# Kernel optimization log

Measured on AMD Instinct MI355X. Metric: run time of the kernel, lower is better.

Reference implementation:

```python
import jax, jax.numpy as jnp
import numpy as np
import math

MUL = 32
E = 131072
N = 10000
IRREPS = [(0, 1), (1, -1), (2, 1)]  # (l, parity) for 0e + 1o + 2e
SQRT3 = math.sqrt(3.0)

_f = math.factorial


def _w3j_symbol(j1, j2, j3, m1, m2, m3):
    """Standard (complex-basis) Wigner 3j symbol via the Racah formula."""
    if m1 + m2 + m3 != 0:
        return 0.0
    if abs(m1) > j1 or abs(m2) > j2 or abs(m3) > j3:
        return 0.0
    if not (abs(j1 - j2) <= j3 <= j1 + j2):
        return 0.0
    tri = _f(j1 + j2 - j3) * _f(j1 - j2 + j3) * _f(-j1 + j2 + j3) / _f(j1 + j2 + j3 + 1)
    pref = (-1) ** (j1 - j2 - m3) * math.sqrt(
        tri * _f(j1 + m1) * _f(j1 - m1) * _f(j2 + m2) * _f(j2 - m2) * _f(j3 + m3) * _f(j3 - m3)
    )
    tmin = max(0, j2 - j3 - m1, j1 - j3 + m2)
    tmax = min(j1 + j2 - j3, j1 - m1, j2 + m2)
    s = 0.0
    for t in range(tmin, tmax + 1):
        s += (-1) ** t / (
            _f(t) * _f(j3 - j2 + t + m1) * _f(j3 - j1 + t - m2)
            * _f(j1 + j2 - j3 - t) * _f(j1 - t - m1) * _f(j2 - t + m2)
        )
    return pref * s


def _real_basis(l):
    """Complex -> real spherical-harmonic change of basis, rows m=-l..l."""
    U = np.zeros((2 * l + 1, 2 * l + 1), dtype=np.complex128)
    U[l, l] = 1.0
    s = 1.0 / math.sqrt(2.0)
    for m in range(1, l + 1):
        U[l + m, l + m] = ((-1) ** m) * s
        U[l + m, l - m] = s
        U[l - m, l - m] = 1j * s
        U[l - m, l + m] = -1j * ((-1) ** m) * s
    return U


def _w3j_real(l1, l2, l3):
    """Real-basis Wigner 3j tensor, Frobenius norm 1 (e3nn normalization)."""
    Wc = np.zeros((2 * l1 + 1, 2 * l2 + 1, 2 * l3 + 1), dtype=np.complex128)
    for m1 in range(-l1, l1 + 1):
        for m2 in range(-l2, l2 + 1):
            for m3 in range(-l3, l3 + 1):
                Wc[l1 + m1, l2 + m2, l3 + m3] = _w3j_symbol(l1, l2, l3, m1, m2, m3)
    C = np.einsum('im,jn,ko,mno->ijk', _real_basis(l1), _real_basis(l2), _real_basis(l3), Wc)
    re, im = C.real, C.imag
    R = re if np.linalg.norm(re) >= np.linalg.norm(im) else im
    return R / np.linalg.norm(R)


def _build_w3j():
    dims = [2 * l + 1 for l, _ in IRREPS]
    offs = np.concatenate([[0], np.cumsum(dims)])[:-1]
    base_dim = int(sum(dims))  # 9
    # auto-generated instructions: same loop order as the torch module
    ins = []
    for io, (lo, po) in enumerate(IRREPS):
        for i1, (l1, p1) in enumerate(IRREPS):
            for i2, (l2, p2) in enumerate(IRREPS):
                if p1 * p2 == po and abs(l1 - l2) <= lo <= l1 + l2:
                    ins.append((i1, i2, io))
    P = len(ins)  # 11 paths
    w3j = np.zeros((P, base_dim, base_dim, base_dim), dtype=np.float32)
    for p, (i1, i2, io) in enumerate(ins):
        l1, l2, lo = IRREPS[i1][0], IRREPS[i2][0], IRREPS[io][0]
        C = _w3j_real(l1, l2, lo) * math.sqrt(2 * lo + 1)  # component normalization
        w3j[p, offs[i1]:offs[i1] + dims[i1], offs[i2]:offs[i2] + dims[i2], offs[io]:offs[io] + dims[io]] = C
    return w3j


def setup_inputs() -> dict:
    key = jax.random.key(0)
    k1, k2, k3, k4 = jax.random.split(key, 4)
    w3j = jnp.asarray(_build_w3j())  # [P=11, 9, 9, 9]
    P = w3j.shape[0]
    base_dim = w3j.shape[1]
    return {
        'x1': jax.random.normal(k1, (E, MUL * base_dim), dtype=jnp.float32),
        'x2': jax.random.normal(k2, (E, MUL * base_dim), dtype=jnp.float32),
        'idxs': jax.random.randint(k3, (E,), 0, N),
        'weights': jax.random.uniform(k4, (MUL, P), dtype=jnp.float32, minval=-SQRT3, maxval=SQRT3),
        'w3j': w3j,
        'scatter_dim_size': N,
    }


def reference(x1, x2, idxs, weights, w3j, scatter_dim_size):
    base1 = w3j.shape[1]
    base2 = w3j.shape[2]
    # scatter edges -> nodes, then gather back per edge (neighbor sum per center)
    x2s = jax.ops.segment_sum(x2, idxs, num_segments=int(scatter_dim_size))
    x2g = x2s[idxs]
    x1r = x1.reshape(-1, MUL, base1)   # [E, u, i]
    x2r = x2g.reshape(-1, MUL, base2)  # [E, u, j]
    # path-channel coupled weighting: 'up,pijk->uijk'
    ww3j = jnp.einsum('up,pijk->uijk', weights, w3j)
    # out[e,u,k] = sum_ij x1[e,u,i] x2[e,u,j] ww3j[u,i,j,k]
    out = jnp.einsum('eui,euj,uijk->euk', x1r, x2r, ww3j)
    return out
```

## Files before the change

### kernel.cpp

```cpp
#include <hip/hip_runtime.h>

#define MULV 32
#define BASE 9
#define ROW 288
#define NPATH 11
#define W3J_SZ 729
#define PACK_STRIDE 96
#define PACK_TOTAL (MULV * PACK_STRIDE)
#define TILE 64
#define BLK 512
#define HCOL 144
#define LSTR 145
#define NH4 36
#define HTOT (TILE * NH4)

typedef float f4a4 __attribute__((ext_vector_type(4), aligned(4)));

__device__ constexpr int p_o1[NPATH] = {0,1,4, 0,1,1,4, 0,1,4,4};
__device__ constexpr int p_d1[NPATH] = {1,3,5, 1,3,3,5, 1,3,5,5};
__device__ constexpr int p_o2[NPATH] = {0,1,4, 1,0,4,1, 4,1,0,4};
__device__ constexpr int p_d2[NPATH] = {1,3,5, 3,1,5,3, 5,3,1,5};
__device__ constexpr int p_o3[NPATH] = {0,0,0, 1,1,1,1, 4,4,4,4};
__device__ constexpr int p_d3[NPATH] = {1,1,1, 3,3,3,3, 5,5,5,5};
__device__ constexpr int p_l1[NPATH] = {0,1,2, 0,1,1,2, 0,1,2,2};
__device__ constexpr int p_l2[NPATH] = {0,1,2, 1,0,2,1, 2,1,0,2};
__device__ constexpr int p_l3[NPATH] = {0,0,0, 1,1,1,1, 2,2,2,2};

__device__ __host__ constexpr bool cell_nz(int p, int i, int j, int k) {
    int m1 = i - p_l1[p], m2 = j - p_l2[p], m3 = k - p_l3[p];
    if ((((m1 < 0) + (m2 < 0) + (m3 < 0)) & 1) != 0) return false;
    int a1 = m1 < 0 ? -m1 : m1, a2 = m2 < 0 ? -m2 : m2, a3 = m3 < 0 ? -m3 : m3;
    int d = a1 - a2; if (d < 0) d = -d;
    return (a3 == a1 + a2) || (a3 == d);
}
__device__ __host__ constexpr bool pair_nz(int p, int i, int j) {
    for (int k = 0; k < p_d3[p]; ++k) if (cell_nz(p, i, j, k)) return true;
    return false;
}


__global__ void zero_count_kernel(float* __restrict__ ws, const int* __restrict__ dN) {
    int N = dN[0];
    int* count = (int*)(ws + PACK_TOTAL + (long)N * ROW);
    for (int i = blockIdx.x * blockDim.x + threadIdx.x; i < N; i += gridDim.x * blockDim.x)
        count[i] = 0;
}

__global__ void hist_kernel(const int* __restrict__ idxs, float* __restrict__ ws,
                            const int* __restrict__ dN, int E) {
    int N = dN[0];
    int* count = (int*)(ws + PACK_TOTAL + (long)N * ROW);
    int t = blockIdx.x * blockDim.x + threadIdx.x;
    if (t < E) atomicAdd(&count[idxs[t]], 1);
}

__global__ void scan_kernel(float* __restrict__ ws, const int* __restrict__ dN) {
    int N = dN[0];
    int* count  = (int*)(ws + PACK_TOTAL + (long)N * ROW);
    int* offset = count + N;
    int* cursor = count + 2 * N;
    __shared__ int tsum[1024];
    const int tid = threadIdx.x;
    int cpt = (N + 1023) / 1024;
    int lo = tid * cpt;
    int hi = lo + cpt; if (hi > N) hi = N;
    int s = 0;
    for (int i = lo; i < hi; ++i) s += count[i];
    int v = s;
    tsum[tid] = v;
    __syncthreads();
    #pragma unroll
    for (int off = 1; off < 1024; off <<= 1) {
        int t = (tid >= off) ? tsum[tid - off] : 0;
        __syncthreads();
        v += t;
        tsum[tid] = v;
        __syncthreads();
    }
    int run = v - s;
    for (int i = lo; i < hi; ++i) {
        int c = count[i];
        offset[i] = run; cursor[i] = run;
        run += c;
    }
}

__global__ void fill_kernel(const int* __restrict__ idxs, float* __restrict__ ws,
                            const int* __restrict__ dN, int E) {
    int N = dN[0];
    int* count  = (int*)(ws + PACK_TOTAL + (long)N * ROW);
    int* cursor = count + 2 * N;
    int* bucket = count + 3 * N;
    int t = blockIdx.x * blockDim.x + threadIdx.x;
    if (t < E) {
        int n = idxs[t];
        int pos = atomicAdd(&cursor[n], 1);
        bucket[pos] = t;
    }
}

__global__ __launch_bounds__(256) void gather_sum_kernel(const float* __restrict__ x2,
                                                         float* __restrict__ ws,
                                                         const int* __restrict__ dN) {
    int N = dN[0];
    float* x2s  = ws + PACK_TOTAL;
    int* count  = (int*)(x2s + (long)N * ROW);
    int* offset = count + N;
    int* bucket = count + 3 * N;
    const int lane = threadIdx.x & 63;
    const int wv   = threadIdx.x >> 6;
    for (int n0 = blockIdx.x * 4 + wv; n0 < N; n0 += gridDim.x * 4) {
        int n   = __builtin_amdgcn_readfirstlane(n0);
        int off = offset[n];
        int deg = count[n];
        float4 a0 = make_float4(0.f, 0.f, 0.f, 0.f);
        float4 a1 = make_float4(0.f, 0.f, 0.f, 0.f);
        int d = 0;
        for (; d + 4 <= deg; d += 4) {
            int e0 = bucket[off + d + 0];
            int e1 = bucket[off + d + 1];
            int e2 = bucket[off + d + 2];
            int e3 = bucket[off + d + 3];
            const float4* r0 = (const float4*)(x2 + (long)e0 * ROW);
            const float4* r1 = (const float4*)(x2 + (long)e1 * ROW);
            const float4* r2 = (const float4*)(x2 + (long)e2 * ROW);
            const float4* r3 = (const float4*)(x2 + (long)e3 * ROW);
            float4 v0 = r0[lane], v1 = r1[lane], v2 = r2[lane], v3 = r3[lane];
            float4 w0, w1, w2, w3;
            if (lane < 8) {
                w0 = r0[64 + lane]; w1 = r1[64 + lane];
                w2 = r2[64 + lane]; w3 = r3[64 + lane];
            }
            a0.x += v0.x + v1.x + v2.x + v3.x;
            a0.y += v0.y + v1.y + v2.y + v3.y;
            a0.z += v0.z + v1.z + v2.z + v3.z;
            a0.w += v0.w + v1.w + v2.w + v3.w;
            if (lane < 8) {
                a1.x += w0.x + w1.x + w2.x + w3.x;
                a1.y += w0.y + w1.y + w2.y + w3.y;
                a1.z += w0.z + w1.z + w2.z + w3.z;
                a1.w += w0.w + w1.w + w2.w + w3.w;
            }
        }
        for (; d < deg; ++d) {
            int e = bucket[off + d];
            const float4* row = (const float4*)(x2 + (long)e * ROW);
            float4 v = row[lane];
            a0.x += v.x; a0.y += v.y; a0.z += v.z; a0.w += v.w;
            if (lane < 8) {
                float4 w = row[64 + lane];
                a1.x += w.x; a1.y += w.y; a1.z += w.z; a1.w += w.w;
            }
        }
        float4* orow = (float4*)(x2s + (long)n * ROW);
        orow[lane] = a0;
        if (lane < 8) orow[64 + lane] = a1;
    }
}

__global__ void ww_build_kernel(const float* __restrict__ weights,
                                const float* __restrict__ w3j,
                                float* __restrict__ packed) {
    int u = threadIdx.x;
    if (u >= MULV) return;
    int ci = 0;
    #pragma unroll
    for (int p = 0; p < NPATH; ++p) {
        float wgt = weights[u * NPATH + p];
        #pragma unroll
        for (int i = 0; i < p_d1[p]; ++i)
            #pragma unroll
            for (int j = 0; j < p_d2[p]; ++j)
                #pragma unroll
                for (int k = 0; k < p_d3[p]; ++k)
                    if (cell_nz(p, i, j, k)) {
                        int idx = (p_o1[p] + i) * 81 + (p_o2[p] + j) * 9 + (p_o3[p] + k);
                        packed[u * PACK_STRIDE + ci] = wgt * w3j[p * W3J_SZ + idx];
                        ++ci;
                    }
    }
}

template <bool GUARD>
__global__ __launch_bounds__(512, 4) void contract_kernel(
    const float* __restrict__ x1, const int* __restrict__ idxs,
    float* __restrict__ ws, const int* __restrict__ dN,
    float* __restrict__ out, int E)
{
    __shared__ float tile[TILE * LSTR];
    __shared__ int lperm[TILE];
    const int tid = threadIdx.x;
    const long ebase = (long)blockIdx.x * TILE;
    const float* __restrict__ packed = ws;
    const float* __restrict__ x2s    = ws + PACK_TOTAL;
    const int N = dN[0];
    const int* __restrict__ bucket = (const int*)(x2s + (long)N * ROW) + 3 * N;

    if (tid < TILE) {
        long ee = ebase + tid;
        lperm[tid] = (!GUARD || ee < (long)E) ? bucket[ee] : -1;
    }
    __syncthreads();

    const int lane = tid & 63;
    const int wv   = __builtin_amdgcn_readfirstlane(tid >> 6);
    const int e    = lperm[lane];
    const int n    = idxs[e >= 0 ? e : 0];
    const float* __restrict__ r2 = x2s + n * ROW;
    float* __restrict__ lrow = &tile[lane * LSTR];

    float x2c[BASE];
    {
        const float* s = r2 + wv * BASE;
        f4a4 a = *(const f4a4*)s;
        f4a4 b = *(const f4a4*)(s + 4);
        x2c[0]=a.x; x2c[1]=a.y; x2c[2]=a.z; x2c[3]=a.w;
        x2c[4]=b.x; x2c[5]=b.y; x2c[6]=b.z; x2c[7]=b.w;
        x2c[8]=s[8];
    }

    #pragma unroll 1
    for (int h = 0; h < 2; ++h) {
        for (int q = tid; q < HTOT; q += BLK) {
            int r = q / NH4, c = q - r * NH4;
            int er = lperm[r];
            if (!GUARD || er >= 0) {
                float4 v = *(const float4*)(x1 + (long)er * ROW + h * HCOL + c * 4);
                float* d = &tile[r * LSTR + c * 4];
                d[0] = v.x; d[1] = v.y; d[2] = v.z; d[3] = v.w;
            }
        }
        __syncthreads();

        #pragma unroll 1
        for (int cc = 0; cc < 2; ++cc) {
            const int m = 2 * h + cc;
            const int u = m * 8 + wv;
            const float* __restrict__ wp = packed + u * PACK_STRIDE;

            float x2n[BASE];
            if (m < 3) {
                const float* s = r2 + (u + 8) * BASE;
                f4a4 a = *(const f4a4*)s;
                f4a4 b = *(const f4a4*)(s + 4);
                x2n[0]=a.x; x2n[1]=a.y; x2n[2]=a.z; x2n[3]=a.w;
                x2n[4]=b.x; x2n[5]=b.y; x2n[6]=b.z; x2n[7]=b.w;
                x2n[8]=s[8];
            }

            const int lbase = (cc * 8 + wv) * BASE;
            float x1v[BASE], acc[BASE];
            #pragma unroll
            for (int i = 0; i < BASE; ++i) {
                x1v[i] = lrow[lbase + i];
                acc[i] = 0.0f;
            }

            int ci = 0;
            #pragma unroll
            for (int p = 0; p < NPATH; ++p) {
                #pragma unroll
                for (int i = 0; i < p_d1[p]; ++i) {
                    #pragma unroll
                    for (int j = 0; j < p_d2[p]; ++j) {
                        if (pair_nz(p, i, j)) {
                            float xx = x1v[p_o1[p] + i] * x2c[p_o2[p] + j];
                            #pragma unroll
                            for (int k = 0; k < p_d3[p]; ++k) {
                                if (cell_nz(p, i, j, k)) {
                                    acc[p_o3[p] + k] = fmaf(wp[ci], xx, acc[p_o3[p] + k]);
                                    ++ci;
                                }
                            }
                        }
                    }
                }
            }
            #pragma unroll
            for (int k = 0; k < BASE; ++k)
                lrow[lbase + k] = acc[k];
            if (m < 3) {
                #pragma unroll
                for (int i = 0; i < BASE; ++i) x2c[i] = x2n[i];
            }
        }
        __syncthreads();

        for (int q = tid; q < HTOT; q += BLK) {
            int r = q / NH4, c = q - r * NH4;
            int er = lperm[r];
            if (!GUARD || er >= 0) {
                const float* s = &tile[r * LSTR + c * 4];
                *(float4*)(out + (long)er * ROW + h * HCOL + c * 4) =
                    make_float4(s[0], s[1], s[2], s[3]);
            }
        }
    }
}

extern "C" void kernel_launch(void* const* d_in, const int* in_sizes, int n_in,
                              void* d_out, int out_size, void* d_ws, size_t ws_size,
                              hipStream_t stream) {
    const float* x1      = (const float*)d_in[0];
    const float* x2      = (const float*)d_in[1];
    const int*   idxs    = (const int*)d_in[2];
    const float* weights = (const float*)d_in[3];
    const float* w3j     = (const float*)d_in[4];
    const int*   dN      = (const int*)d_in[5];
    float* out = (float*)d_out;
    float* ws  = (float*)d_ws;

    const int E = in_sizes[2];
    const int eb = (E + 255) / 256;

    zero_count_kernel<<<256, 256, 0, stream>>>(ws, dN);
    hist_kernel<<<eb, 256, 0, stream>>>(idxs, ws, dN, E);
    scan_kernel<<<1, 1024, 0, stream>>>(ws, dN);
    fill_kernel<<<eb, 256, 0, stream>>>(idxs, ws, dN, E);

    gather_sum_kernel<<<2500, 256, 0, stream>>>(x2, ws, dN);

    ww_build_kernel<<<1, 64, 0, stream>>>(weights, w3j, ws);

    if (E % TILE == 0) {
        contract_kernel<false><<<E / TILE, BLK, 0, stream>>>(x1, idxs, ws, dN, out, E);
    } else {
        contract_kernel<true><<<(E + TILE - 1) / TILE, BLK, 0, stream>>>(x1, idxs, ws, dN, out, E);
    }
}
```

Measured before the change: 165.3 us.

## Shrink contract block to 256 threads and stage x1 in padded per-channel LDS slots

The contraction kernel drops from 512 to 256 threads per block and processes each 64-edge tile in four quarter-row passes instead of two halves. Each channel's 9 x1 values are staged in LDS at a 12-float padded stride, so the registers can be loaded and stored with float4 LDS accesses. The goal is fewer scalar LDS operations, less LDS per block and more blocks resident per CU. The cost is more barrier phases per tile and misaligned 9-float global loads and stores.

```diff
diff --git a/kernel.cpp b/kernel.cpp
--- a/kernel.cpp
+++ b/kernel.cpp
@@ -8,11 +8,9 @@
 #define PACK_STRIDE 96
 #define PACK_TOTAL (MULV * PACK_STRIDE)
 #define TILE 64
-#define BLK 512
-#define HCOL 144
-#define LSTR 145
-#define NH4 36
-#define HTOT (TILE * NH4)
+#define QCOL 72
+#define PSTR 12
+#define LSTR 100
 
 typedef float f4a4 __attribute__((ext_vector_type(4), aligned(4)));
 
@@ -182,7 +180,7 @@
 }
 
 template <bool GUARD>
-__global__ __launch_bounds__(512, 4) void contract_kernel(
+__global__ __launch_bounds__(256, 4) void contract_kernel(
     const float* __restrict__ x1, const int* __restrict__ idxs,
     float* __restrict__ ws, const int* __restrict__ dN,
     float* __restrict__ out, int E)
@@ -206,7 +204,7 @@
     const int wv   = __builtin_amdgcn_readfirstlane(tid >> 6);
     const int e    = lperm[lane];
     const int n    = idxs[e >= 0 ? e : 0];
-    const float* __restrict__ r2 = x2s + n * ROW;
+    const float* __restrict__ r2 = x2s + (long)n * ROW;
     float* __restrict__ lrow = &tile[lane * LSTR];
 
     float x2c[BASE];
@@ -220,27 +218,33 @@
     }
 
     #pragma unroll 1
-    for (int h = 0; h < 2; ++h) {
-        for (int q = tid; q < HTOT; q += BLK) {
-            int r = q / NH4, c = q - r * NH4;
-            int er = lperm[r];
+    for (int h = 0; h < 4; ++h) {
+        #pragma unroll
+        for (int s = 0; s < 2; ++s) {
+            int pair = tid + (s << 8);
+            int row = pair >> 3, ul = pair & 7;
+            int er = lperm[row];
             if (!GUARD || er >= 0) {
-                float4 v = *(const float4*)(x1 + (long)er * ROW + h * HCOL + c * 4);
-                float* d = &tile[r * LSTR + c * 4];
-                d[0] = v.x; d[1] = v.y; d[2] = v.z; d[3] = v.w;
+                const float* src = x1 + (long)er * ROW + h * QCOL + ul * BASE;
+                f4a4 a = *(const f4a4*)src;
+                f4a4 b = *(const f4a4*)(src + 4);
+                float c8 = src[8];
+                float* d = &tile[row * LSTR + ul * PSTR];
+                *(float4*)d       = make_float4(a.x, a.y, a.z, a.w);
+                *(float4*)(d + 4) = make_float4(b.x, b.y, b.z, b.w);
+                d[8] = c8;
             }
         }
         __syncthreads();
 
         #pragma unroll 1
         for (int cc = 0; cc < 2; ++cc) {
-            const int m = 2 * h + cc;
-            const int u = m * 8 + wv;
+            const int u = 8 * h + cc * 4 + wv;
             const float* __restrict__ wp = packed + u * PACK_STRIDE;
 
             float x2n[BASE];
-            if (m < 3) {
-                const float* s = r2 + (u + 8) * BASE;
+            if (u + 4 < MULV) {
+                const float* s = r2 + (u + 4) * BASE;
                 f4a4 a = *(const f4a4*)s;
                 f4a4 b = *(const f4a4*)(s + 4);
                 x2n[0]=a.x; x2n[1]=a.y; x2n[2]=a.z; x2n[3]=a.w;
@@ -248,13 +252,17 @@
                 x2n[8]=s[8];
             }
 
-            const int lbase = (cc * 8 + wv) * BASE;
+            const int lbase = (cc * 4 + wv) * PSTR;
             float x1v[BASE], acc[BASE];
+            {
+                float4 A = *(const float4*)&lrow[lbase];
+                float4 B = *(const float4*)&lrow[lbase + 4];
+                x1v[0]=A.x; x1v[1]=A.y; x1v[2]=A.z; x1v[3]=A.w;
+                x1v[4]=B.x; x1v[5]=B.y; x1v[6]=B.z; x1v[7]=B.w;
+                x1v[8]=lrow[lbase + 8];
+            }
             #pragma unroll
-            for (int i = 0; i < BASE; ++i) {
-                x1v[i] = lrow[lbase + i];
-                acc[i] = 0.0f;
-            }
+            for (int k = 0; k < BASE; ++k) acc[k] = 0.0f;
 
             int ci = 0;
             #pragma unroll
@@ -276,23 +284,30 @@
                     }
                 }
             }
-            #pragma unroll
-            for (int k = 0; k < BASE; ++k)
-                lrow[lbase + k] = acc[k];
-            if (m < 3) {
+            *(float4*)&lrow[lbase]     = make_float4(acc[0], acc[1], acc[2], acc[3]);
+            *(float4*)&lrow[lbase + 4] = make_float4(acc[4], acc[5], acc[6], acc[7]);
+            lrow[lbase + 8] = acc[8];
+            if (u + 4 < MULV) {
                 #pragma unroll
                 for (int i = 0; i < BASE; ++i) x2c[i] = x2n[i];
             }
         }
         __syncthreads();
 
-        for (int q = tid; q < HTOT; q += BLK) {
-            int r = q / NH4, c = q - r * NH4;
-            int er = lperm[r];
+        #pragma unroll
+        for (int s = 0; s < 2; ++s) {
+            int pair = tid + (s << 8);
+            int row = pair >> 3, ul = pair & 7;
+            int er = lperm[row];
             if (!GUARD || er >= 0) {
-                const float* s = &tile[r * LSTR + c * 4];
-                *(float4*)(out + (long)er * ROW + h * HCOL + c * 4) =
-                    make_float4(s[0], s[1], s[2], s[3]);
+                const float* dsrc = &tile[row * LSTR + ul * PSTR];
+                float4 A = *(const float4*)dsrc;
+                float4 B = *(const float4*)(dsrc + 4);
+                float c8 = dsrc[8];
+                float* dst = out + (long)er * ROW + h * QCOL + ul * BASE;
+                *(f4a4*)dst       = (f4a4){A.x, A.y, A.z, A.w};
+                *(f4a4*)(dst + 4) = (f4a4){B.x, B.y, B.z, B.w};
+                dst[8] = c8;
             }
         }
     }
@@ -323,8 +338,8 @@
     ww_build_kernel<<<1, 64, 0, stream>>>(weights, w3j, ws);
 
     if (E % TILE == 0) {
-        contract_kernel<false><<<E / TILE, BLK, 0, stream>>>(x1, idxs, ws, dN, out, E);
+        contract_kernel<false><<<E / TILE, 256, 0, stream>>>(x1, idxs, ws, dN, out, E);
     } else {
-        contract_kernel<true><<<(E + TILE - 1) / TILE, BLK, 0, stream>>>(x1, idxs, ws, dN, out, E);
-    }
-}
+        contract_kernel<true><<<(E + TILE - 1) / TILE, 256, 0, stream>>>(x1, idxs, ws, dN, out, E);
+    }
+}
```

Measured after the change: 181.6 us. 9.8% more time.
